# Kernel tuning notes

Hardware: AMD Instinct MI355X
Metric: run time of the kernel (lower is better)

## Reference

```python
import jax, jax.numpy as jnp
import numpy as np

N, P, C, H, W = 2, 100, 256, 128, 192
K = 3; KK = K * K; E = C * KK; NH = 8; DH = E // NH; FFN = 2048


def _ln(x, g, b, eps=1e-5):
    m = x.mean(-1, keepdims=True)
    v = ((x - m) ** 2).mean(-1, keepdims=True)
    return (x - m) * jax.lax.rsqrt(v + eps) * g + b


def setup_inputs():
    ks = iter(jax.random.split(jax.random.key(0), 64))
    def rnd(shape, s=1.0):
        return jax.random.normal(next(ks), shape, jnp.float32) * s
    z = lambda *s: jnp.zeros(s, jnp.float32)
    o = lambda *s: jnp.ones(s, jnp.float32)
    return {
        'x': rnd((N, C, H, W)),
        'proposal_feat': rnd((N, P, E)),
        'mask_preds': rnd((N, P, H, W)),
        'ku_dyn_w': rnd((2 * C, C), 0.02), 'ku_dyn_b': z(2 * C),
        'ku_in_w': rnd((2 * C, C), 0.02), 'ku_in_b': z(2 * C),
        'ku_ig_w': rnd((C, C), 0.02), 'ku_ig_b': z(C),
        'ku_ug_w': rnd((C, C), 0.02), 'ku_ug_b': z(C),
        'ku_nin_g': o(C), 'ku_nin_b': z(C),
        'ku_nout_g': o(C), 'ku_nout_b': z(C),
        'ku_inin_g': o(C), 'ku_inin_b': z(C),
        'ku_inout_g': o(C), 'ku_inout_b': z(C),
        'ku_fc_w': rnd((C, C), 0.02), 'ku_fc_b': z(C),
        'ku_fcn_g': o(C), 'ku_fcn_b': z(C),
        'attn_in_w': rnd((3 * E, E), 0.02), 'attn_in_b': z(3 * E),
        'attn_out_w': rnd((E, E), 0.02), 'attn_out_b': z(E),
        'attn_ln_g': o(E), 'attn_ln_b': z(E),
        'ffn_w1': rnd((FFN, C), 0.02), 'ffn_b1': z(FFN),
        'ffn_w2': rnd((C, FFN), 0.02), 'ffn_b2': z(C),
        'ffn_ln_g': o(C), 'ffn_ln_b': z(C),
        'mask_fc_ws': rnd((3, C, C), 0.02),
        'mask_fc_ln_g': o(3, C), 'mask_fc_ln_b': z(3, C),
        'fc_mask_w': rnd((C, C), 0.02), 'fc_mask_b': z(C),
    }


def _forward(x, proposal_feat, mask_preds, ku_dyn_w, ku_dyn_b, ku_in_w, ku_in_b,
             ku_ig_w, ku_ig_b, ku_ug_w, ku_ug_b, ku_nin_g, ku_nin_b, ku_nout_g,
             ku_nout_b, ku_inin_g, ku_inin_b, ku_inout_g, ku_inout_b, ku_fc_w,
             ku_fc_b, ku_fcn_g, ku_fcn_b, attn_in_w, attn_in_b, attn_out_w,
             attn_out_b, attn_ln_g, attn_ln_b, ffn_w1, ffn_b1, ffn_w2, ffn_b2,
             ffn_ln_g, ffn_ln_b, mask_fc_ws, mask_fc_ln_g, mask_fc_ln_b,
             fc_mask_w, fc_mask_b):
    # mask-softmax pooling over proposals: (N,P,H,W) x (N,C,H,W) -> (N,P,C)
    sig = jax.nn.softmax(mask_preds, axis=1)
    x_feat = jnp.einsum('bnhw,bchw->bnc', sig, x)

    # KernelUpdator (gated dynamic kernel update)
    pf = proposal_feat.reshape(N, P, C, KK).transpose(0, 1, 3, 2).reshape(N * P, KK, C)
    upd = x_feat.reshape(N * P, C)
    params = upd @ ku_dyn_w.T + ku_dyn_b            # (NP, 2C)
    p_in, p_out = params[:, :C], params[:, C:]
    inp = pf @ ku_in_w.T + ku_in_b                  # (NP, KK, 2C)
    i_in, i_out = inp[..., :C], inp[..., C:]
    gate = i_in * p_in[:, None, :]                  # (NP, KK, C)
    ig = jax.nn.sigmoid(_ln(gate @ ku_ig_w.T + ku_ig_b, ku_inin_g, ku_inin_b))
    ug = jax.nn.sigmoid(_ln(gate @ ku_ug_w.T + ku_ug_b, ku_nin_g, ku_nin_b))
    p_out = _ln(p_out, ku_nout_g, ku_nout_b)
    i_out = _ln(i_out, ku_inout_g, ku_inout_b)
    feat = ug * p_out[:, None, :] + ig * i_out
    feat = jax.nn.relu(_ln(feat @ ku_fc_w.T + ku_fc_b, ku_fcn_g, ku_fcn_b))  # (NP,KK,C)

    # self-attention across proposals; embed dim E = C*K*K, with residual + LN
    obj = feat.reshape(N, P, E).transpose(1, 0, 2)  # (P,N,E)
    qkv = obj @ attn_in_w.T + attn_in_b
    q, k, v = jnp.split(qkv, 3, axis=-1)
    q = q.reshape(P, N, NH, DH) * np.float32(1.0 / np.sqrt(DH))
    k = k.reshape(P, N, NH, DH)
    v = v.reshape(P, N, NH, DH)
    a = jax.nn.softmax(jnp.einsum('qnhd,knhd->nhqk', q, k), axis=-1)
    o = jnp.einsum('nhqk,knhd->qnhd', a, v).reshape(P, N, E)
    obj = _ln(obj + o @ attn_out_w.T + attn_out_b, attn_ln_g, attn_ln_b)
    obj = obj.transpose(1, 0, 2).reshape(N, P, KK, C)

    # FFN (residual) + LN, applied per (proposal, kernel position)
    h = jax.nn.relu(obj @ ffn_w1.T + ffn_b1) @ ffn_w2.T + ffn_b2
    obj = _ln(obj + h, ffn_ln_g, ffn_ln_b)

    mf = obj
    for i in range(3):
        mf = jax.nn.relu(_ln(mf @ mask_fc_ws[i].T, mask_fc_ln_g[i], mask_fc_ln_b[i]))
    mf = mf @ fc_mask_w.T + fc_mask_b               # (N,P,KK,C)
    kernels = mf.transpose(0, 1, 3, 2).reshape(N, P, C, K, K)

    # per-image dynamic conv: vmap replaces the python loop over batch
    def conv_one(xi, wi):
        return jax.lax.conv_general_dilated(
            xi[None], wi, (1, 1), 'SAME',
            dimension_numbers=('NCHW', 'OIHW', 'NCHW'))[0]
    new_masks = jax.vmap(conv_one)(x, kernels)      # (N,P,H,W)

    obj_kernels = obj.transpose(0, 1, 3, 2).reshape(N, P, C, K, K)
    return new_masks, obj_kernels


def reference(x, proposal_feat, mask_preds, ku_dyn_w, ku_dyn_b, ku_in_w, ku_in_b,
              ku_ig_w, ku_ig_b, ku_ug_w, ku_ug_b, ku_nin_g, ku_nin_b, ku_nout_g,
              ku_nout_b, ku_inin_g, ku_inin_b, ku_inout_g, ku_inout_b, ku_fc_w,
              ku_fc_b, ku_fcn_g, ku_fcn_b, attn_in_w, attn_in_b, attn_out_w,
              attn_out_b, attn_ln_g, attn_ln_b, ffn_w1, ffn_b1, ffn_w2, ffn_b2,
              ffn_ln_g, ffn_ln_b, mask_fc_ws, mask_fc_ln_g, mask_fc_ln_b,
              fc_mask_w, fc_mask_b):
    return _forward(x, proposal_feat, mask_preds, ku_dyn_w, ku_dyn_b, ku_in_w,
                    ku_in_b, ku_ig_w, ku_ig_b, ku_ug_w, ku_ug_b, ku_nin_g,
                    ku_nin_b, ku_nout_g, ku_nout_b, ku_inin_g, ku_inin_b,
                    ku_inout_g, ku_inout_b, ku_fc_w, ku_fc_b, ku_fcn_g, ku_fcn_b,
                    attn_in_w, attn_in_b, attn_out_w, attn_out_b, attn_ln_g,
                    attn_ln_b, ffn_w1, ffn_b1, ffn_w2, ffn_b2, ffn_ln_g,
                    ffn_ln_b, mask_fc_ws, mask_fc_ln_g, mask_fc_ln_b,
                    fc_mask_w, fc_mask_b)
```

## Files before the change

kernel.cpp:

```cpp
#include <hip/hip_runtime.h>
#include <hip/hip_bf16.h>

#define N_ 2
#define P_ 100
#define C_ 256
#define H_ 128
#define W_ 192
#define HW_ 24576
#define KK_ 9
#define E_ 2304
#define NH_ 8
#define DH_ 288
#define FFN_ 2048
#define NP_ 200
#define ROWS_ 1800
#define XKC_ 64

typedef __attribute__((ext_vector_type(8))) __bf16 bf16x8;
typedef __attribute__((ext_vector_type(4))) float f32x4;

__global__ __launch_bounds__(256) void k_softmax(const float* __restrict__ mp, float* __restrict__ sig){
  int idx = blockIdx.x*256 + threadIdx.x;
  if(idx >= N_*HW_) return;
  int n = idx / HW_, hw = idx - n*HW_;
  const float* base = mp + (size_t)n*P_*HW_ + hw;
  float m = -1e30f;
  for(int p=0;p<P_;p++) m = fmaxf(m, base[(size_t)p*HW_]);
  float s = 0.f;
  for(int p=0;p<P_;p++) s += __expf(base[(size_t)p*HW_] - m);
  float inv = 1.f/s;
  float* ob = sig + (size_t)n*P_*HW_ + hw;
  for(int p=0;p<P_;p++) ob[(size_t)p*HW_] = __expf(base[(size_t)p*HW_] - m)*inv;
}

__global__ __launch_bounds__(256) void k_permute_pf(const float* __restrict__ prop, float* __restrict__ pf){
  int i = blockIdx.x*256 + threadIdx.x;
  if(i >= ROWS_*C_) return;
  int c = i & 255;
  int r = i >> 8;
  int kk = r % 9, np = r / 9;
  pf[i] = prop[(size_t)np*E_ + c*KK_ + kk];
}

__global__ __launch_bounds__(256) void k_xfeat1m(const float* __restrict__ sig, const float* __restrict__ x,
                                                 float* __restrict__ partial){
  const int ct = blockIdx.x, kb = blockIdx.y, n = blockIdx.z;
  const int hw0 = kb*384;
  const int tid = threadIdx.x;
  const int wid = tid >> 6, lane = tid & 63;
  const int col = lane & 15, quad = lane >> 4;
  const int wm = wid & 1, wn = wid >> 1;
  const int MT = wm ? 3 : 4;
  __shared__ __bf16 As[112][72];
  __shared__ __bf16 Bs[128][72];
  f32x4 acc[4][4] = {};
  for(int k0=0; k0<384; k0+=64){
    __syncthreads();
    for(int i=tid; i<896; i+=256){
      int p = i >> 3, kg = i & 7;
      bf16x8 v;
      if(p < P_){
        const float* sp = &sig[((size_t)n*P_ + p)*HW_ + hw0 + k0 + kg*8];
        const float4 f0 = *(const float4*)sp;
        const float4 f1 = *(const float4*)(sp+4);
        v[0]=(__bf16)f0.x; v[1]=(__bf16)f0.y; v[2]=(__bf16)f0.z; v[3]=(__bf16)f0.w;
        v[4]=(__bf16)f1.x; v[5]=(__bf16)f1.y; v[6]=(__bf16)f1.z; v[7]=(__bf16)f1.w;
      } else {
        #pragma unroll
        for(int u=0;u<8;u++) v[u] = (__bf16)0.f;
      }
      *(bf16x8*)&As[p][kg*8] = v;
    }
    for(int i=tid; i<1024; i+=256){
      int c = i >> 3, kg = i & 7;
      const float* xp = &x[((size_t)n*C_ + ct*128 + c)*HW_ + hw0 + k0 + kg*8];
      const float4 f0 = *(const float4*)xp;
      const float4 f1 = *(const float4*)(xp+4);
      bf16x8 v;
      v[0]=(__bf16)f0.x; v[1]=(__bf16)f0.y; v[2]=(__bf16)f0.z; v[3]=(__bf16)f0.w;
      v[4]=(__bf16)f1.x; v[5]=(__bf16)f1.y; v[6]=(__bf16)f1.z; v[7]=(__bf16)f1.w;
      *(bf16x8*)&Bs[c][kg*8] = v;
    }
    __syncthreads();
    #pragma unroll
    for(int ks=0; ks<2; ks++){
      bf16x8 b[4];
      #pragma unroll
      for(int t=0;t<4;t++) b[t] = *(const bf16x8*)&Bs[(wn*4+t)*16 + col][ks*32 + quad*8];
      #pragma unroll
      for(int mt=0; mt<4; mt++){
        if(mt < MT){
          bf16x8 a = *(const bf16x8*)&As[(wm*4+mt)*16 + col][ks*32 + quad*8];
          #pragma unroll
          for(int t=0;t<4;t++)
            acc[mt][t] = __builtin_amdgcn_mfma_f32_16x16x32_bf16(a, b[t], acc[mt][t], 0, 0, 0);
        }
      }
    }
  }
  #pragma unroll
  for(int mt=0; mt<4; mt++){
    if(mt < MT){
      #pragma unroll
      for(int r=0;r<4;r++){
        int p = (wm*4+mt)*16 + quad*4 + r;
        if(p < P_){
          float* op = &partial[(((size_t)n*XKC_ + kb)*P_ + p)*C_ + ct*128 + wn*64 + col];
          #pragma unroll
          for(int t=0;t<4;t++) op[t*16] = acc[mt][t][r];
        }
      }
    }
  }
}

__global__ __launch_bounds__(256) void k_xfeat2(const float* __restrict__ partial, float* __restrict__ xfeat){
  int np = blockIdx.x;
  int n = np / P_, p = np - n*P_;
  int c = threadIdx.x;
  float s = 0.f;
  for(int kb=0;kb<XKC_;kb++) s += partial[(((size_t)n*XKC_ + kb)*P_ + p)*C_ + c];
  xfeat[(size_t)np*C_ + c] = s;
}

__global__ __launch_bounds__(256) void k_gemm_mfma(const float* __restrict__ A, const float* __restrict__ Wt,
    const float* __restrict__ bias, float* __restrict__ out, int M, int N, int K, int act)
{
  const int n0 = blockIdx.x*128, m0 = blockIdx.y*64;
  const int tid = threadIdx.x;
  const int wid = tid >> 6, lane = tid & 63;
  const int col = lane & 15, quad = lane >> 4;
  const int wm = wid & 1, wn = wid >> 1;
  __shared__ __bf16 As[64][72];
  __shared__ __bf16 Bs[128][72];
  f32x4 acc[2][4] = {};
  for(int k0=0; k0<K; k0+=64){
    __syncthreads();
    for(int i=tid; i<512; i+=256){
      int r = i >> 3, kg = i & 7;
      int m = m0 + r;
      bf16x8 v;
      if(m < M){
        const float* ap = &A[(size_t)m*K + k0 + kg*8];
        const float4 f0 = *(const float4*)ap;
        const float4 f1 = *(const float4*)(ap+4);
        v[0]=(__bf16)f0.x; v[1]=(__bf16)f0.y; v[2]=(__bf16)f0.z; v[3]=(__bf16)f0.w;
        v[4]=(__bf16)f1.x; v[5]=(__bf16)f1.y; v[6]=(__bf16)f1.z; v[7]=(__bf16)f1.w;
      } else {
        #pragma unroll
        for(int u=0;u<8;u++) v[u] = (__bf16)0.f;
      }
      *(bf16x8*)&As[r][kg*8] = v;
    }
    for(int i=tid; i<1024; i+=256){
      int r = i >> 3, kg = i & 7;
      const float* wp = &Wt[(size_t)(n0 + r)*K + k0 + kg*8];
      const float4 f0 = *(const float4*)wp;
      const float4 f1 = *(const float4*)(wp+4);
      bf16x8 v;
      v[0]=(__bf16)f0.x; v[1]=(__bf16)f0.y; v[2]=(__bf16)f0.z; v[3]=(__bf16)f0.w;
      v[4]=(__bf16)f1.x; v[5]=(__bf16)f1.y; v[6]=(__bf16)f1.z; v[7]=(__bf16)f1.w;
      *(bf16x8*)&Bs[r][kg*8] = v;
    }
    __syncthreads();
    #pragma unroll
    for(int ks=0; ks<2; ks++){
      bf16x8 b[4], a[2];
      #pragma unroll
      for(int t=0;t<4;t++) b[t] = *(const bf16x8*)&Bs[(wn*4+t)*16 + col][ks*32 + quad*8];
      #pragma unroll
      for(int mt=0;mt<2;mt++) a[mt] = *(const bf16x8*)&As[(wm*2+mt)*16 + col][ks*32 + quad*8];
      #pragma unroll
      for(int mt=0;mt<2;mt++)
        #pragma unroll
        for(int t=0;t<4;t++)
          acc[mt][t] = __builtin_amdgcn_mfma_f32_16x16x32_bf16(a[mt], b[t], acc[mt][t], 0, 0, 0);
    }
  }
  #pragma unroll
  for(int mt=0;mt<2;mt++){
    #pragma unroll
    for(int r=0;r<4;r++){
      int m = m0 + (wm*2+mt)*16 + quad*4 + r;
      if(m < M){
        #pragma unroll
        for(int t=0;t<4;t++){
          int n = n0 + (wn*4+t)*16 + col;
          float v = acc[mt][t][r];
          if(bias) v += bias[n];
          if(act == 1) v = fmaxf(v, 0.f);
          if(act == 3) ((__bf16*)out)[(size_t)m*N + n] = (__bf16)v;
          else out[(size_t)m*N + n] = v;
        }
      }
    }
  }
}

__global__ __launch_bounds__(256) void k_gemm_splitk(const float* __restrict__ A, const float* __restrict__ Wt,
    float* __restrict__ part, int M, int N, int K, int KC)
{
  const int n0 = blockIdx.x*128, m0 = blockIdx.y*64;
  const int kz = blockIdx.z*KC;
  const int tid = threadIdx.x;
  const int wid = tid >> 6, lane = tid & 63;
  const int col = lane & 15, quad = lane >> 4;
  const int wm = wid & 1, wn = wid >> 1;
  __shared__ __bf16 As[64][72];
  __shared__ __bf16 Bs[128][72];
  f32x4 acc[2][4] = {};
  for(int k0=kz; k0<kz+KC; k0+=64){
    __syncthreads();
    for(int i=tid; i<512; i+=256){
      int r = i >> 3, kg = i & 7;
      int m = m0 + r;
      bf16x8 v;
      if(m < M){
        const float* ap = &A[(size_t)m*K + k0 + kg*8];
        const float4 f0 = *(const float4*)ap;
        const float4 f1 = *(const float4*)(ap+4);
        v[0]=(__bf16)f0.x; v[1]=(__bf16)f0.y; v[2]=(__bf16)f0.z; v[3]=(__bf16)f0.w;
        v[4]=(__bf16)f1.x; v[5]=(__bf16)f1.y; v[6]=(__bf16)f1.z; v[7]=(__bf16)f1.w;
      } else {
        #pragma unroll
        for(int u=0;u<8;u++) v[u] = (__bf16)0.f;
      }
      *(bf16x8*)&As[r][kg*8] = v;
    }
    for(int i=tid; i<1024; i+=256){
      int r = i >> 3, kg = i & 7;
      const float* wp = &Wt[(size_t)(n0 + r)*K + k0 + kg*8];
      const float4 f0 = *(const float4*)wp;
      const float4 f1 = *(const float4*)(wp+4);
      bf16x8 v;
      v[0]=(__bf16)f0.x; v[1]=(__bf16)f0.y; v[2]=(__bf16)f0.z; v[3]=(__bf16)f0.w;
      v[4]=(__bf16)f1.x; v[5]=(__bf16)f1.y; v[6]=(__bf16)f1.z; v[7]=(__bf16)f1.w;
      *(bf16x8*)&Bs[r][kg*8] = v;
    }
    __syncthreads();
    #pragma unroll
    for(int ks=0; ks<2; ks++){
      bf16x8 b[4], a[2];
      #pragma unroll
      for(int t=0;t<4;t++) b[t] = *(const bf16x8*)&Bs[(wn*4+t)*16 + col][ks*32 + quad*8];
      #pragma unroll
      for(int mt=0;mt<2;mt++) a[mt] = *(const bf16x8*)&As[(wm*2+mt)*16 + col][ks*32 + quad*8];
      #pragma unroll
      for(int mt=0;mt<2;mt++)
        #pragma unroll
        for(int t=0;t<4;t++)
          acc[mt][t] = __builtin_amdgcn_mfma_f32_16x16x32_bf16(a[mt], b[t], acc[mt][t], 0, 0, 0);
    }
  }
  float* pbase = part + (size_t)blockIdx.z*M*N;
  #pragma unroll
  for(int mt=0;mt<2;mt++){
    #pragma unroll
    for(int r=0;r<4;r++){
      int m = m0 + (wm*2+mt)*16 + quad*4 + r;
      if(m < M){
        #pragma unroll
        for(int t=0;t<4;t++){
          int n = n0 + (wn*4+t)*16 + col;
          pbase[(size_t)m*N + n] = acc[mt][t][r];
        }
      }
    }
  }
}

__global__ __launch_bounds__(256) void k_redk(const float* __restrict__ part, const float* __restrict__ bias,
    float* __restrict__ out, int M, int N, int S)
{
  size_t i4 = ((size_t)blockIdx.x*256 + threadIdx.x)*4;
  size_t MN = (size_t)M*N;
  if(i4 >= MN) return;
  float4 s = *(const float4*)&part[i4];
  for(int z=1; z<S; z++){
    const float4 p = *(const float4*)&part[(size_t)z*MN + i4];
    s.x+=p.x; s.y+=p.y; s.z+=p.z; s.w+=p.w;
  }
  if(bias){
    int n = (int)(i4 % (size_t)N);
    const float4 b = *(const float4*)&bias[n];
    s.x+=b.x; s.y+=b.y; s.z+=b.z; s.w+=b.w;
  }
  *(float4*)&out[i4] = s;
}

__global__ __launch_bounds__(256) void k_ln256(const float* __restrict__ in, const float* __restrict__ res,
    const float* __restrict__ g, const float* __restrict__ b, float* __restrict__ out, int M, int act)
{
  int row = blockIdx.x*4 + (threadIdx.x >> 6);
  int lane = threadIdx.x & 63;
  if(row >= M) return;
  float4 v = *(const float4*)&in[(size_t)row*C_ + lane*4];
  if(res){
    const float4 rv = *(const float4*)&res[(size_t)row*C_ + lane*4];
    v.x += rv.x; v.y += rv.y; v.z += rv.z; v.w += rv.w;
  }
  float s = v.x + v.y + v.z + v.w;
  float q = v.x*v.x + v.y*v.y + v.z*v.z + v.w*v.w;
  #pragma unroll
  for(int off=32; off; off>>=1){ s += __shfl_xor(s, off, 64); q += __shfl_xor(q, off, 64); }
  float mean = s*(1.f/256.f);
  float rstd = rsqrtf(q*(1.f/256.f) - mean*mean + 1e-5f);
  const float4 gv = *(const float4*)&g[lane*4];
  const float4 bv = *(const float4*)&b[lane*4];
  float o[4] = {(v.x-mean)*rstd*gv.x + bv.x, (v.y-mean)*rstd*gv.y + bv.y,
                (v.z-mean)*rstd*gv.z + bv.z, (v.w-mean)*rstd*gv.w + bv.w};
  #pragma unroll
  for(int j=0;j<4;j++){
    if(act==1) o[j] = fmaxf(o[j], 0.f);
    else if(act==2) o[j] = 1.f/(1.f + __expf(-o[j]));
  }
  float4 ov = {o[0],o[1],o[2],o[3]};
  *(float4*)&out[(size_t)row*C_ + lane*4] = ov;
}

__global__ __launch_bounds__(256) void k_gate(const float* __restrict__ inp, const float* __restrict__ params,
                                              float* __restrict__ gate){
  int i = blockIdx.x*256 + threadIdx.x;
  if(i >= ROWS_*C_) return;
  int c = i & 255, r = i >> 8;
  int np = r / 9;
  gate[i] = inp[(size_t)r*512 + c] * params[(size_t)np*512 + c];
}

__device__ __forceinline__ void block_stats(float v, float* red, int slot, float& mean, float& rstd){
  float s = v, q = v*v;
  #pragma unroll
  for(int off=32; off; off>>=1){ s += __shfl_xor(s, off, 64); q += __shfl_xor(q, off, 64); }
  int wid = threadIdx.x >> 6;
  if((threadIdx.x & 63) == 0){ red[slot + wid] = s; red[slot + 4 + wid] = q; }
  __syncthreads();
  s = red[slot+0]+red[slot+1]+red[slot+2]+red[slot+3];
  q = red[slot+4]+red[slot+5]+red[slot+6]+red[slot+7];
  mean = s*(1.f/256.f);
  rstd = rsqrtf(q*(1.f/256.f) - mean*mean + 1e-5f);
}

__global__ __launch_bounds__(256) void k_combine(const float* __restrict__ params, const float* __restrict__ inp,
  const float* __restrict__ ug, const float* __restrict__ ig,
  const float* __restrict__ nout_g, const float* __restrict__ nout_b,
  const float* __restrict__ inout_g, const float* __restrict__ inout_b,
  float* __restrict__ feat)
{
  __shared__ float red[16];
  int r = blockIdx.x;
  int np = r / 9;
  int c = threadIdx.x;
  float pv = params[(size_t)np*512 + 256 + c];
  float mean, rstd;
  block_stats(pv, red, 0, mean, rstd);
  float pn = (pv - mean)*rstd*nout_g[c] + nout_b[c];
  float iv = inp[(size_t)r*512 + 256 + c];
  float mean2, rstd2;
  block_stats(iv, red, 8, mean2, rstd2);
  float iw = (iv - mean2)*rstd2*inout_g[c] + inout_b[c];
  size_t o = (size_t)r*C_ + c;
  feat[o] = ug[o]*pn + ig[o]*iw;
}

__global__ __launch_bounds__(256) void k_attn2(const float* __restrict__ qkv, float* __restrict__ attnO){
  const int qt = blockIdx.x, h = blockIdx.y, n = blockIdx.z;
  const int q0 = qt*10;
  const int tid = threadIdx.x;
  __shared__ float Qs[10][292];
  __shared__ float KVs[25][292];
  __shared__ float Ss[10][104];
  const float scale = 0.05892556509887896f;
  const size_t base = (size_t)n*P_*6912 + (size_t)h*DH_;
  for(int i=tid; i<10*DH_; i+=256){
    int qi = i/DH_, d = i - qi*DH_;
    Qs[qi][d] = qkv[base + (size_t)(q0+qi)*6912 + d] * scale;
  }
  for(int kt=0; kt<4; kt++){
    int kp0 = kt*25;
    __syncthreads();
    for(int i=tid; i<25*DH_; i+=256){
      int ki = i/DH_, d = i - ki*DH_;
      KVs[ki][d] = qkv[base + (size_t)(kp0+ki)*6912 + E_ + d];
    }
    __syncthreads();
    if(tid < 250){
      int qi = tid/25, ki = tid - qi*25;
      float s = 0.f;
      #pragma unroll 9
      for(int d=0; d<DH_; d+=4){
        const float4 a = *(const float4*)&Qs[qi][d];
        const float4 b = *(const float4*)&KVs[ki][d];
        s += a.x*b.x + a.y*b.y + a.z*b.z + a.w*b.w;
      }
      Ss[qi][kp0+ki] = s;
    }
  }
  __syncthreads();
  {
    int w = tid >> 6, lane = tid & 63;
    for(int r=w; r<10; r+=4){
      float v0 = (lane < 100) ? Ss[r][lane] : -1e30f;
      float v1 = (lane < 36)  ? Ss[r][64+lane] : -1e30f;
      float m = fmaxf(v0, v1);
      #pragma unroll
      for(int off=32; off; off>>=1) m = fmaxf(m, __shfl_xor(m, off, 64));
      float e0 = (lane < 100) ? __expf(v0-m) : 0.f;
      float e1 = (lane < 36)  ? __expf(v1-m) : 0.f;
      float s = e0 + e1;
      #pragma unroll
      for(int off=32; off; off>>=1) s += __shfl_xor(s, off, 64);
      float inv = 1.f/s;
      if(lane < 100) Ss[r][lane] = e0*inv;
      if(lane < 36)  Ss[r][64+lane] = e1*inv;
    }
  }
  float acc[12];
  #pragma unroll
  for(int j=0;j<12;j++) acc[j]=0.f;
  for(int kt=0; kt<4; kt++){
    int kp0 = kt*25;
    __syncthreads();
    for(int i=tid; i<25*DH_; i+=256){
      int ki = i/DH_, d = i - ki*DH_;
      KVs[ki][d] = qkv[base + (size_t)(kp0+ki)*6912 + 2*E_ + d];
    }
    __syncthreads();
    int j = 0;
    for(int i=tid; i<10*DH_; i+=256, j++){
      int qi = i/DH_, d = i - qi*DH_;
      float s = acc[j];
      #pragma unroll
      for(int ki=0; ki<25; ki++) s += Ss[qi][kp0+ki]*KVs[ki][d];
      acc[j] = s;
    }
  }
  {
    int j = 0;
    for(int i=tid; i<10*DH_; i+=256, j++){
      int qi = i/DH_, d = i - qi*DH_;
      attnO[(size_t)(n*P_ + q0 + qi)*E_ + h*DH_ + d] = acc[j];
    }
  }
}

__global__ __launch_bounds__(256) void k_add_ln2304(const float* __restrict__ obj0, const float* __restrict__ tp,
  const float* __restrict__ g, const float* __restrict__ b, float* __restrict__ out)
{
  __shared__ float red[8];
  int row = blockIdx.x;
  float v[9]; float s=0.f, q=0.f;
  #pragma unroll
  for(int j=0;j<9;j++){
    int e = threadIdx.x + j*256;
    float t = obj0[(size_t)row*E_ + e] + tp[(size_t)row*E_ + e];
    v[j]=t; s+=t; q+=t*t;
  }
  #pragma unroll
  for(int off=32; off; off>>=1){ s += __shfl_xor(s, off, 64); q += __shfl_xor(q, off, 64); }
  int wid = threadIdx.x>>6;
  if((threadIdx.x&63)==0){ red[wid]=s; red[4+wid]=q; }
  __syncthreads();
  s = red[0]+red[1]+red[2]+red[3]; q = red[4]+red[5]+red[6]+red[7];
  float mean = s*(1.f/2304.f);
  float rstd = rsqrtf(q*(1.f/2304.f) - mean*mean + 1e-5f);
  #pragma unroll
  for(int j=0;j<9;j++){
    int e = threadIdx.x + j*256;
    out[(size_t)row*E_ + e] = (v[j]-mean)*rstd*g[e] + b[e];
  }
}

__global__ __launch_bounds__(256) void k_objk(const float* __restrict__ obj2, float* __restrict__ outk){
  int i = blockIdx.x*256 + threadIdx.x;
  if(i >= ROWS_*C_) return;
  int kk = i % 9; int t = i / 9; int c = t & 255; int np = t >> 8;
  outk[i] = obj2[((size_t)np*9 + kk)*C_ + c];
}

__global__ __launch_bounds__(256) void k_prep_x(const float* __restrict__ x, __bf16* __restrict__ xT){
  int i = blockIdx.x*256 + threadIdx.x;
  if(i >= N_*32*H_*W_) return;
  int w = i % W_; int t = i / W_;
  int h = t % H_; t /= H_;
  int g = t % 32; int n = t / 32;
  const float* xp = &x[((size_t)(n*C_ + g*8)*H_ + h)*W_ + w];
  bf16x8 v;
  #pragma unroll
  for(int u=0;u<8;u++) v[u] = (__bf16)xp[(size_t)u*HW_];
  *(bf16x8*)&xT[(size_t)i*8] = v;
}

__global__ __launch_bounds__(256) void k_conv_mfma(const __bf16* __restrict__ xT, const __bf16* __restrict__ kerb,
                                                   float* __restrict__ out){
  const int wt = blockIdx.x, ht = blockIdx.y, z = blockIdx.z;
  const int n = z >> 1, ps = z & 1;
  const int pbase = ps*64;
  const int NT = ps ? 3 : 4;
  const int tid = threadIdx.x;
  const int hi = tid >> 6;
  const int lane = tid & 63;
  const int col = lane & 15, quad = lane >> 4;
  const int w0 = wt*64, h0 = ht*4;

  __shared__ __bf16 xs[6][4][66][8];
  __shared__ __bf16 ks[9][4][64][8];

  f32x4 acc[4][4] = {};

  for(int c0=0; c0<C_; c0+=32){
    __syncthreads();
    for(int i=tid; i<1584; i+=256){
      int oct = i / 396;
      int rem = i - oct*396;
      int hy = rem / 66, wx = rem - hy*66;
      int hh = h0 - 1 + hy, ww = w0 - 1 + wx;
      bf16x8 v;
      if(hh >= 0 && hh < H_ && ww >= 0 && ww < W_){
        v = *(const bf16x8*)&xT[((((size_t)n*32 + (c0>>3) + oct)*H_ + hh)*W_ + ww)*8];
      } else {
        #pragma unroll
        for(int u=0;u<8;u++) v[u] = (__bf16)0.f;
      }
      *(bf16x8*)&xs[hy][oct][wx][0] = v;
    }
    for(int i=tid; i<2304; i+=256){
      int oct = i / 576;
      int r2 = i - oct*576;
      int tap = r2 >> 6, pl = r2 & 63;
      int p = pbase + pl;
      bf16x8 v;
      if(p < P_){
        v = *(const bf16x8*)&kerb[((size_t)(n*P_+p)*9 + tap)*C_ + c0 + oct*8];
      } else {
        #pragma unroll
        for(int u=0;u<8;u++) v[u] = (__bf16)0.f;
      }
      *(bf16x8*)&ks[tap][oct][pl][0] = v;
    }
    __syncthreads();
    #pragma unroll
    for(int ky=0; ky<3; ky++){
      #pragma unroll
      for(int kx=0; kx<3; kx++){
        const int tap = ky*3 + kx;
        const int hy = hi + ky;
        bf16x8 b[4];
        #pragma unroll
        for(int t=0;t<4;t++) b[t] = *(const bf16x8*)&xs[hy][quad][t*16 + col + kx][0];
        #pragma unroll
        for(int pt=0; pt<4; pt++){
          if(pt < NT){
            bf16x8 a = *(const bf16x8*)&ks[tap][quad][pt*16 + col][0];
            #pragma unroll
            for(int t=0;t<4;t++)
              acc[pt][t] = __builtin_amdgcn_mfma_f32_16x16x32_bf16(a, b[t], acc[pt][t], 0, 0, 0);
          }
        }
      }
    }
  }
  const int h = h0 + hi;
  #pragma unroll
  for(int pt=0; pt<4; pt++){
    if(pt < NT){
      #pragma unroll
      for(int r=0;r<4;r++){
        int p = pbase + pt*16 + quad*4 + r;
        if(p < P_){
          float* op = &out[((size_t)(n*P_+p)*H_ + h)*W_ + w0 + col];
          #pragma unroll
          for(int t=0;t<4;t++) op[t*16] = acc[pt][t][r];
        }
      }
    }
  }
}

extern "C" void kernel_launch(void* const* d_in, const int* in_sizes, int n_in,
                              void* d_out, int out_size, void* d_ws, size_t ws_size,
                              hipStream_t stream)
{
  (void)in_sizes; (void)n_in; (void)out_size; (void)ws_size;
  const float* x          = (const float*)d_in[0];
  const float* prop       = (const float*)d_in[1];
  const float* mask_pred  = (const float*)d_in[2];
  const float* ku_dyn_w   = (const float*)d_in[3];
  const float* ku_dyn_b   = (const float*)d_in[4];
  const float* ku_in_w    = (const float*)d_in[5];
  const float* ku_in_b    = (const float*)d_in[6];
  const float* ku_ig_w    = (const float*)d_in[7];
  const float* ku_ig_b    = (const float*)d_in[8];
  const float* ku_ug_w    = (const float*)d_in[9];
  const float* ku_ug_b    = (const float*)d_in[10];
  const float* ku_nin_g   = (const float*)d_in[11];
  const float* ku_nin_b   = (const float*)d_in[12];
  const float* ku_nout_g  = (const float*)d_in[13];
  const float* ku_nout_b  = (const float*)d_in[14];
  const float* ku_inin_g  = (const float*)d_in[15];
  const float* ku_inin_b  = (const float*)d_in[16];
  const float* ku_inout_g = (const float*)d_in[17];
  const float* ku_inout_b = (const float*)d_in[18];
  const float* ku_fc_w    = (const float*)d_in[19];
  const float* ku_fc_b    = (const float*)d_in[20];
  const float* ku_fcn_g   = (const float*)d_in[21];
  const float* ku_fcn_b   = (const float*)d_in[22];
  const float* attn_in_w  = (const float*)d_in[23];
  const float* attn_in_b  = (const float*)d_in[24];
  const float* attn_out_w = (const float*)d_in[25];
  const float* attn_out_b = (const float*)d_in[26];
  const float* attn_ln_g  = (const float*)d_in[27];
  const float* attn_ln_b  = (const float*)d_in[28];
  const float* ffn_w1     = (const float*)d_in[29];
  const float* ffn_b1     = (const float*)d_in[30];
  const float* ffn_w2     = (const float*)d_in[31];
  const float* ffn_b2     = (const float*)d_in[32];
  const float* ffn_ln_g   = (const float*)d_in[33];
  const float* ffn_ln_b   = (const float*)d_in[34];
  const float* mask_fc_ws = (const float*)d_in[35];
  const float* mask_fc_ln_g = (const float*)d_in[36];
  const float* mask_fc_ln_b = (const float*)d_in[37];
  const float* fc_mask_w  = (const float*)d_in[38];
  const float* fc_mask_b  = (const float*)d_in[39];

  float* ws = (float*)d_ws;
  float* sig     = ws;
  float* hbuf    = ws;
  float* skA     = ws;
  float* partial = ws + 4915200;
  float* qkv     = ws + 4915200;
  float* skB     = ws + 4915200;
  float* attnO   = ws + 4915200 + 1382400;
  float* tproj   = ws + 4915200 + 1843200;
  float* tmp     = ws + 4915200 + 2304000;
  float* xfeat   = ws + 9830400;
  float* params  = xfeat + 51200;
  float* pf      = params + 102400;
  float* inp     = pf + 460800;
  float* gate    = inp + 921600;
  float* ig      = gate + 460800;
  float* ug      = ig + 460800;
  float* feat    = ug + 460800;
  float* obj0    = feat + 460800;
  float* obj1    = obj0 + 460800;
  float* obj2    = obj1 + 460800;
  float* mf1     = obj2 + 460800;
  float* mf2     = mf1 + 460800;
  float* mfF     = mf2 + 460800;
  __bf16* xT = (__bf16*)ws;

  float* out_masks = (float*)d_out;
  float* out_kern  = out_masks + (size_t)N_*P_*HW_;

  k_softmax<<<192, 256, 0, stream>>>(mask_pred, sig);
  k_permute_pf<<<1800, 256, 0, stream>>>(prop, pf);
  k_xfeat1m<<<dim3(2,XKC_,2), 256, 0, stream>>>(sig, x, partial);
  k_xfeat2<<<200, 256, 0, stream>>>(partial, xfeat);
  k_gemm_mfma<<<dim3(4,4),   256, 0, stream>>>(xfeat, ku_dyn_w, ku_dyn_b, params, 200, 512, 256, 0);
  k_gemm_mfma<<<dim3(4,29),  256, 0, stream>>>(pf, ku_in_w, ku_in_b, inp, 1800, 512, 256, 0);
  k_gate<<<1800, 256, 0, stream>>>(inp, params, gate);
  k_gemm_mfma<<<dim3(2,29),  256, 0, stream>>>(gate, ku_ig_w, ku_ig_b, tmp, 1800, 256, 256, 0);
  k_ln256<<<450, 256, 0, stream>>>(tmp, nullptr, ku_inin_g, ku_inin_b, ig, 1800, 2);
  k_gemm_mfma<<<dim3(2,29),  256, 0, stream>>>(gate, ku_ug_w, ku_ug_b, tmp, 1800, 256, 256, 0);
  k_ln256<<<450, 256, 0, stream>>>(tmp, nullptr, ku_nin_g, ku_nin_b, ug, 1800, 2);
  k_combine<<<1800, 256, 0, stream>>>(params, inp, ug, ig, ku_nout_g, ku_nout_b, ku_inout_g, ku_inout_b, feat);
  k_gemm_mfma<<<dim3(2,29),  256, 0, stream>>>(feat, ku_fc_w, ku_fc_b, tmp, 1800, 256, 256, 0);
  k_ln256<<<450, 256, 0, stream>>>(tmp, nullptr, ku_fcn_g, ku_fcn_b, obj0, 1800, 1);
  k_gemm_splitk<<<dim3(54,4,3), 256, 0, stream>>>(obj0, attn_in_w, skA, 200, 6912, 2304, 768);
  k_redk<<<1350, 256, 0, stream>>>(skA, attn_in_b, qkv, 200, 6912, 3);
  k_attn2<<<dim3(10,8,2), 256, 0, stream>>>(qkv, attnO);
  k_gemm_splitk<<<dim3(18,4,4), 256, 0, stream>>>(attnO, attn_out_w, skA, 200, 2304, 2304, 576);
  k_redk<<<450, 256, 0, stream>>>(skA, attn_out_b, tproj, 200, 2304, 4);
  k_add_ln2304<<<200, 256, 0, stream>>>(obj0, tproj, attn_ln_g, attn_ln_b, obj1);
  k_gemm_mfma<<<dim3(16,29), 256, 0, stream>>>(obj1, ffn_w1, ffn_b1, hbuf, 1800, 2048, 256, 1);
  k_gemm_splitk<<<dim3(2,29,4), 256, 0, stream>>>(hbuf, ffn_w2, skB, 1800, 256, 2048, 512);
  k_redk<<<450, 256, 0, stream>>>(skB, ffn_b2, tmp, 1800, 256, 4);
  k_ln256<<<450, 256, 0, stream>>>(tmp, obj1, ffn_ln_g, ffn_ln_b, obj2, 1800, 0);
  k_gemm_mfma<<<dim3(2,29),  256, 0, stream>>>(obj2, mask_fc_ws,          nullptr, tmp, 1800, 256, 256, 0);
  k_ln256<<<450, 256, 0, stream>>>(tmp, nullptr, mask_fc_ln_g,       mask_fc_ln_b,       mf1, 1800, 1);
  k_gemm_mfma<<<dim3(2,29),  256, 0, stream>>>(mf1,  mask_fc_ws + 65536,  nullptr, tmp, 1800, 256, 256, 0);
  k_ln256<<<450, 256, 0, stream>>>(tmp, nullptr, mask_fc_ln_g + 256, mask_fc_ln_b + 256, mf2, 1800, 1);
  k_gemm_mfma<<<dim3(2,29),  256, 0, stream>>>(mf2,  mask_fc_ws + 131072, nullptr, tmp, 1800, 256, 256, 0);
  k_ln256<<<450, 256, 0, stream>>>(tmp, nullptr, mask_fc_ln_g + 512, mask_fc_ln_b + 512, mf1, 1800, 1);
  k_gemm_mfma<<<dim3(2,29),  256, 0, stream>>>(mf1, fc_mask_w, fc_mask_b, mfF, 1800, 256, 256, 3);
  k_objk<<<1800, 256, 0, stream>>>(obj2, out_kern);
  k_prep_x<<<6144, 256, 0, stream>>>(x, xT);
  k_conv_mfma<<<dim3(3,32,4), 256, 0, stream>>>(xT, (const __bf16*)mfF, out_masks);
}
```

Baseline: 739.4 us.

## Use full-M split-K GEMM, XCD-aware panel mapping, and pre-permuted conv kernels

Adds a split-K GEMM variant whose block covers all 256 rows of M, so each weight tile is loaded once for the attention in/out projections. The out projection now splits K nine ways. The FFN2 split-K GEMM gets a 1D grid remapped so blocks sharing a weight panel land on the same XCD for L2 reuse. The dynamic conv kernel weights are pre-permuted into a contiguous per-chunk layout, so the conv kernel's shared-memory load becomes a straight copy. The costs are an extra permute launch, more partial-sum traffic for the 9-way split, and a large per-block accumulator and LDS footprint that lowers occupancy.

```diff
diff --git a/kernel.cpp b/kernel.cpp
--- a/kernel.cpp
+++ b/kernel.cpp
@@ -197,11 +197,89 @@
   }
 }
 
-__global__ __launch_bounds__(256) void k_gemm_splitk(const float* __restrict__ A, const float* __restrict__ Wt,
+__global__ __launch_bounds__(256) void k_gemm_skM256(const float* __restrict__ A, const float* __restrict__ Wt,
     float* __restrict__ part, int M, int N, int K, int KC)
 {
-  const int n0 = blockIdx.x*128, m0 = blockIdx.y*64;
-  const int kz = blockIdx.z*KC;
+  const int n0 = blockIdx.x*128;
+  const int kz = blockIdx.y*KC;
+  const int tid = threadIdx.x;
+  const int wid = tid >> 6, lane = tid & 63;
+  const int col = lane & 15, quad = lane >> 4;
+  const int wm = wid & 1, wn = wid >> 1;
+  __shared__ __bf16 As[256][72];
+  __shared__ __bf16 Bs[128][72];
+  f32x4 acc[8][4] = {};
+  for(int k0=kz; k0<kz+KC; k0+=64){
+    __syncthreads();
+    for(int i=tid; i<2048; i+=256){
+      int r = i >> 3, kg = i & 7;
+      bf16x8 v;
+      if(r < M){
+        const float* ap = &A[(size_t)r*K + k0 + kg*8];
+        const float4 f0 = *(const float4*)ap;
+        const float4 f1 = *(const float4*)(ap+4);
+        v[0]=(__bf16)f0.x; v[1]=(__bf16)f0.y; v[2]=(__bf16)f0.z; v[3]=(__bf16)f0.w;
+        v[4]=(__bf16)f1.x; v[5]=(__bf16)f1.y; v[6]=(__bf16)f1.z; v[7]=(__bf16)f1.w;
+      } else {
+        #pragma unroll
+        for(int u=0;u<8;u++) v[u] = (__bf16)0.f;
+      }
+      *(bf16x8*)&As[r][kg*8] = v;
+    }
+    for(int i=tid; i<1024; i+=256){
+      int r = i >> 3, kg = i & 7;
+      const float* wp = &Wt[(size_t)(n0 + r)*K + k0 + kg*8];
+      const float4 f0 = *(const float4*)wp;
+      const float4 f1 = *(const float4*)(wp+4);
+      bf16x8 v;
+      v[0]=(__bf16)f0.x; v[1]=(__bf16)f0.y; v[2]=(__bf16)f0.z; v[3]=(__bf16)f0.w;
+      v[4]=(__bf16)f1.x; v[5]=(__bf16)f1.y; v[6]=(__bf16)f1.z; v[7]=(__bf16)f1.w;
+      *(bf16x8*)&Bs[r][kg*8] = v;
+    }
+    __syncthreads();
+    #pragma unroll
+    for(int ks=0; ks<2; ks++){
+      bf16x8 b[4];
+      #pragma unroll
+      for(int t=0;t<4;t++) b[t] = *(const bf16x8*)&Bs[(wn*4+t)*16 + col][ks*32 + quad*8];
+      #pragma unroll
+      for(int mt=0;mt<8;mt++){
+        bf16x8 a = *(const bf16x8*)&As[(wm*8+mt)*16 + col][ks*32 + quad*8];
+        #pragma unroll
+        for(int t=0;t<4;t++)
+          acc[mt][t] = __builtin_amdgcn_mfma_f32_16x16x32_bf16(a, b[t], acc[mt][t], 0, 0, 0);
+      }
+    }
+  }
+  float* pbase = part + (size_t)blockIdx.y*M*N;
+  #pragma unroll
+  for(int mt=0;mt<8;mt++){
+    #pragma unroll
+    for(int r=0;r<4;r++){
+      int m = (wm*8+mt)*16 + quad*4 + r;
+      if(m < M){
+        #pragma unroll
+        for(int t=0;t<4;t++){
+          int n = n0 + (wn*4+t)*16 + col;
+          pbase[(size_t)m*N + n] = acc[mt][t][r];
+        }
+      }
+    }
+  }
+}
+
+__global__ __launch_bounds__(256) void k_gemm_splitk(const float* __restrict__ A, const float* __restrict__ Wt,
+    float* __restrict__ part, int M, int N, int K, int KC, int PX, int MY)
+{
+  const int wg = blockIdx.x;
+  const int xcd = wg & 7, slot = wg >> 3;
+  const int mb = slot % MY, pg = slot / MY;
+  const int panel = xcd + 8*pg;
+  const int PZ = K / KC;
+  if(panel >= PX*PZ) return;
+  const int px = panel % PX, pz = panel / PX;
+  const int n0 = px*128, m0 = mb*64;
+  const int kz = pz*KC;
   const int tid = threadIdx.x;
   const int wid = tid >> 6, lane = tid & 63;
   const int col = lane & 15, quad = lane >> 4;
@@ -252,7 +330,7 @@
           acc[mt][t] = __builtin_amdgcn_mfma_f32_16x16x32_bf16(a[mt], b[t], acc[mt][t], 0, 0, 0);
     }
   }
-  float* pbase = part + (size_t)blockIdx.z*M*N;
+  float* pbase = part + (size_t)pz*M*N;
   #pragma unroll
   for(int mt=0;mt<2;mt++){
     #pragma unroll
@@ -490,7 +568,26 @@
   *(bf16x8*)&xT[(size_t)i*8] = v;
 }
 
-__global__ __launch_bounds__(256) void k_conv_mfma(const __bf16* __restrict__ xT, const __bf16* __restrict__ kerb,
+__global__ __launch_bounds__(256) void k_permute_ker(const __bf16* __restrict__ mfFb, __bf16* __restrict__ kerP){
+  int i = blockIdx.x*256 + threadIdx.x;
+  if(i >= 73728) return;
+  int pl = i & 63; int t = i >> 6;
+  int oct = t & 3; t >>= 2;
+  int tap = t % 9; t /= 9;
+  int c0b = t & 7; int nps = t >> 3;
+  int n = nps >> 1, ps = nps & 1;
+  int p = ps*64 + pl;
+  bf16x8 v;
+  if(p < P_){
+    v = *(const bf16x8*)&mfFb[((size_t)(n*P_+p)*9 + tap)*C_ + c0b*32 + oct*8];
+  } else {
+    #pragma unroll
+    for(int u=0;u<8;u++) v[u] = (__bf16)0.f;
+  }
+  *(bf16x8*)&kerP[(size_t)i*8] = v;
+}
+
+__global__ __launch_bounds__(256) void k_conv_mfma(const __bf16* __restrict__ xT, const __bf16* __restrict__ kerP,
                                                    float* __restrict__ out){
   const int wt = blockIdx.x, ht = blockIdx.y, z = blockIdx.z;
   const int n = z >> 1, ps = z & 1;
@@ -504,6 +601,7 @@
 
   __shared__ __bf16 xs[6][4][66][8];
   __shared__ __bf16 ks[9][4][64][8];
+  __bf16* ksf = &ks[0][0][0][0];
 
   f32x4 acc[4][4] = {};
 
@@ -523,19 +621,10 @@
       }
       *(bf16x8*)&xs[hy][oct][wx][0] = v;
     }
-    for(int i=tid; i<2304; i+=256){
-      int oct = i / 576;
-      int r2 = i - oct*576;
-      int tap = r2 >> 6, pl = r2 & 63;
-      int p = pbase + pl;
-      bf16x8 v;
-      if(p < P_){
-        v = *(const bf16x8*)&kerb[((size_t)(n*P_+p)*9 + tap)*C_ + c0 + oct*8];
-      } else {
-        #pragma unroll
-        for(int u=0;u<8;u++) v[u] = (__bf16)0.f;
-      }
-      *(bf16x8*)&ks[tap][oct][pl][0] = v;
+    {
+      const __bf16* kp = kerP + ((size_t)(n*2+ps)*8 + (c0>>5))*2304*8;
+      for(int i=tid; i<2304; i+=256)
+        *(bf16x8*)&ksf[(size_t)i*8] = *(const bf16x8*)&kp[(size_t)i*8];
     }
     __syncthreads();
     #pragma unroll
@@ -647,6 +736,7 @@
   float* mf2     = mf1 + 460800;
   float* mfF     = mf2 + 460800;
   __bf16* xT = (__bf16*)ws;
+  __bf16* kerP = (__bf16*)(ws + 6758400);
 
   float* out_masks = (float*)d_out;
   float* out_kern  = out_masks + (size_t)N_*P_*HW_;
@@ -665,14 +755,14 @@
   k_combine<<<1800, 256, 0, stream>>>(params, inp, ug, ig, ku_nout_g, ku_nout_b, ku_inout_g, ku_inout_b, feat);
   k_gemm_mfma<<<dim3(2,29),  256, 0, stream>>>(feat, ku_fc_w, ku_fc_b, tmp, 1800, 256, 256, 0);
   k_ln256<<<450, 256, 0, stream>>>(tmp, nullptr, ku_fcn_g, ku_fcn_b, obj0, 1800, 1);
-  k_gemm_splitk<<<dim3(54,4,3), 256, 0, stream>>>(obj0, attn_in_w, skA, 200, 6912, 2304, 768);
+  k_gemm_skM256<<<dim3(54,3), 256, 0, stream>>>(obj0, attn_in_w, skA, 200, 6912, 2304, 768);
   k_redk<<<1350, 256, 0, stream>>>(skA, attn_in_b, qkv, 200, 6912, 3);
   k_attn2<<<dim3(10,8,2), 256, 0, stream>>>(qkv, attnO);
-  k_gemm_splitk<<<dim3(18,4,4), 256, 0, stream>>>(attnO, attn_out_w, skA, 200, 2304, 2304, 576);
-  k_redk<<<450, 256, 0, stream>>>(skA, attn_out_b, tproj, 200, 2304, 4);
+  k_gemm_skM256<<<dim3(18,9), 256, 0, stream>>>(attnO, attn_out_w, skA, 200, 2304, 2304, 256);
+  k_redk<<<450, 256, 0, stream>>>(skA, attn_out_b, tproj, 200, 2304, 9);
   k_add_ln2304<<<200, 256, 0, stream>>>(obj0, tproj, attn_ln_g, attn_ln_b, obj1);
   k_gemm_mfma<<<dim3(16,29), 256, 0, stream>>>(obj1, ffn_w1, ffn_b1, hbuf, 1800, 2048, 256, 1);
-  k_gemm_splitk<<<dim3(2,29,4), 256, 0, stream>>>(hbuf, ffn_w2, skB, 1800, 256, 2048, 512);
+  k_gemm_splitk<<<232, 256, 0, stream>>>(hbuf, ffn_w2, skB, 1800, 256, 2048, 512, 2, 29);
   k_redk<<<450, 256, 0, stream>>>(skB, ffn_b2, tmp, 1800, 256, 4);
   k_ln256<<<450, 256, 0, stream>>>(tmp, obj1, ffn_ln_g, ffn_ln_b, obj2, 1800, 0);
   k_gemm_mfma<<<dim3(2,29),  256, 0, stream>>>(obj2, mask_fc_ws,          nullptr, tmp, 1800, 256, 256, 0);
@@ -683,6 +773,7 @@
   k_ln256<<<450, 256, 0, stream>>>(tmp, nullptr, mask_fc_ln_g + 512, mask_fc_ln_b + 512, mf1, 1800, 1);
   k_gemm_mfma<<<dim3(2,29),  256, 0, stream>>>(mf1, fc_mask_w, fc_mask_b, mfF, 1800, 256, 256, 3);
   k_objk<<<1800, 256, 0, stream>>>(obj2, out_kern);
+  k_permute_ker<<<288, 256, 0, stream>>>((const __bf16*)mfF, kerP);
   k_prep_x<<<6144, 256, 0, stream>>>(x, xT);
-  k_conv_mfma<<<dim3(3,32,4), 256, 0, stream>>>(xT, (const __bf16*)mfF, out_masks);
-}
+  k_conv_mfma<<<dim3(3,32,4), 256, 0, stream>>>(xT, kerP, out_masks);
+}
```

After: 763.3 us. +3.2%, slower.
